# Optimization experiments

Measured on AMD Instinct MI355X. Metric: run time of the kernel, lower is better.

The kernel has to match this reference:

```python
import jax, jax.numpy as jnp
import numpy as np

C_CURV = 0.01
K = 20
BALL_EPS = 4e-3  # hyptorch float32 boundary eps


def _e2p(x, c=C_CURV):
    # ToPoincare: expmap0 then project onto the Poincare ball
    sqrt_c = c ** 0.5
    n = jnp.maximum(jnp.linalg.norm(x, axis=-1, keepdims=True), 1e-15)
    y = jnp.tanh(sqrt_c * n) * x / (sqrt_c * n)
    maxnorm = (1.0 - BALL_EPS) / sqrt_c
    ny = jnp.maximum(jnp.linalg.norm(y, axis=-1, keepdims=True), 1e-15)
    return jnp.where(ny > maxnorm, y * (maxnorm / ny), y)


def _mobius_add(x, y, c=C_CURV):
    x2 = jnp.sum(x * x, axis=-1, keepdims=True)
    y2 = jnp.sum(y * y, axis=-1, keepdims=True)
    xy = jnp.sum(x * y, axis=-1, keepdims=True)
    num = (1.0 + 2.0 * c * xy + c * y2) * x + (1.0 - c * x2) * y
    den = 1.0 + 2.0 * c * xy + c * c * x2 * y2
    return num / jnp.maximum(den, 1e-15)


def _knn(x, k):
    # x: (B, C, N); Euclidean negative squared distance, topk indices
    inner = -2.0 * jnp.einsum('bcn,bcm->bnm', x, x)
    xx = jnp.sum(x * x, axis=1)  # (B, N)
    pd = -xx[:, :, None] - inner - xx[:, None, :]
    return jax.lax.top_k(pd, k)[1]  # (B, N, k)


def _graph_feature(x, k=K):
    # x: (B, C, N) -> (B, 2C, N, k)
    idx = _knn(x, k)
    xp = _e2p(jnp.transpose(x, (0, 2, 1)))  # (B, N, C) on Poincare ball
    feat = jax.vmap(lambda xb, ib: xb[ib])(xp, idx)  # (B, N, k, C) gather
    xc = jnp.broadcast_to(xp[:, :, None, :], feat.shape)
    out = jnp.concatenate([_mobius_add(feat, -xc), xc], axis=-1)
    return jnp.transpose(out, (0, 3, 1, 2))


def _bn(x, g, b, axes, eps=1e-5):
    # BatchNorm (training-mode batch statistics), channel axis = 1
    m = jnp.mean(x, axis=axes, keepdims=True)
    v = jnp.mean((x - m) ** 2, axis=axes, keepdims=True)
    shp = [1] * x.ndim
    shp[1] = -1
    return (x - m) / jnp.sqrt(v + eps) * g.reshape(shp) + b.reshape(shp)


def _ln(x, g, b, eps=1e-5):
    m = jnp.mean(x, axis=-1, keepdims=True)
    v = jnp.mean((x - m) ** 2, axis=-1, keepdims=True)
    return (x - m) / jnp.sqrt(v + eps) * g + b


def setup_inputs() -> dict:
    key = jax.random.key(0)
    ks = jax.random.split(key, 8)
    B, N, OUT = 16, 1024, 40
    s = 0.05
    return {
        'x': jax.random.normal(ks[0], (B, N, 3), jnp.float32),
        'conv1_w': jax.random.normal(ks[1], (64, 6), jnp.float32) * s,
        'bn1_g': jnp.ones((64,), jnp.float32), 'bn1_b': jnp.zeros((64,), jnp.float32),
        'conv2_w': jax.random.normal(ks[2], (192, 128), jnp.float32) * s,
        'bn2_g': jnp.ones((192,), jnp.float32), 'bn2_b': jnp.zeros((192,), jnp.float32),
        'conv3_w': jax.random.normal(ks[3], (1024, 256), jnp.float32) * s,
        'bn3_g': jnp.ones((1024,), jnp.float32), 'bn3_b': jnp.zeros((1024,), jnp.float32),
        'fc1_w': jax.random.normal(ks[4], (512, 1024), jnp.float32) * s,
        'fc1_b': jnp.zeros((512,), jnp.float32),
        'ln1_g': jnp.ones((512,), jnp.float32), 'ln1_b': jnp.zeros((512,), jnp.float32),
        'fc2_w': jax.random.normal(ks[5], (256, 512), jnp.float32) * s,
        'fc2_b': jnp.zeros((256,), jnp.float32),
        'ln2_g': jnp.ones((256,), jnp.float32), 'ln2_b': jnp.zeros((256,), jnp.float32),
        'out_w': jax.random.normal(ks[6], (OUT, 256), jnp.float32) * s,
        'out_b': jnp.zeros((OUT,), jnp.float32),
    }


def reference(x, conv1_w, bn1_g, bn1_b, conv2_w, bn2_g, bn2_b,
              conv3_w, bn3_g, bn3_b, fc1_w, fc1_b, ln1_g, ln1_b,
              fc2_w, fc2_b, ln2_g, ln2_b, out_w, out_b):
    xt = jnp.transpose(x, (0, 2, 1))  # (B, 3, N)
    f = _graph_feature(xt)            # (B, 6, N, k)
    h = jnp.einsum('oc,bcnk->bonk', conv1_w, f)
    h = jax.nn.relu(_bn(h, bn1_g, bn1_b, (0, 2, 3)))
    x1 = jnp.max(h, axis=-1)          # (B, 64, N)
    f = _graph_feature(x1)            # (B, 128, N, k)
    h = jnp.einsum('oc,bcnk->bonk', conv2_w, f)
    h = jax.nn.relu(_bn(h, bn2_g, bn2_b, (0, 2, 3)))
    x2 = jnp.max(h, axis=-1)          # (B, 192, N)
    h = jnp.concatenate([x1, x2], axis=1)  # (B, 256, N)
    h = jnp.einsum('oc,bcn->bon', conv3_w, h)
    h = jax.nn.relu(_bn(h, bn3_g, bn3_b, (0, 2)))
    h = jnp.max(h, axis=-1)           # (B, 1024)
    h = jax.nn.relu(_ln(h @ fc1_w.T + fc1_b, ln1_g, ln1_b))
    h = jax.nn.relu(_ln(h @ fc2_w.T + fc2_b, ln2_g, ln2_b))
    logits = h @ out_w.T + out_b      # (B, outdim)
    return jax.nn.log_softmax(logits, axis=1)
```

## Files before the change

kernel.cpp:

```cpp
#include <hip/hip_runtime.h>
#include <math.h>

#define B_ 16
#define N_ 1024
#define KNN 20
#define NPAIR (B_*N_)

typedef __attribute__((ext_vector_type(8))) short bf16x8;
typedef __attribute__((ext_vector_type(4))) float f32x4;

__device__ __forceinline__ unsigned fkey(float f) {
  unsigned u = __float_as_uint(f);
  return (u & 0x80000000u) ? ~u : (u | 0x80000000u);
}
__device__ __forceinline__ float fkeyinv(unsigned u) {
  unsigned b = (u & 0x80000000u) ? (u ^ 0x80000000u) : ~u;
  return __uint_as_float(b);
}
__device__ __forceinline__ unsigned short f2bf(float x) {
  unsigned u = __float_as_uint(x);
  unsigned r = (u + 0x7FFFu + ((u >> 16) & 1u)) >> 16;
  return (unsigned short)r;
}
__device__ __forceinline__ float bf2f(unsigned short u) {
  return __uint_as_float(((unsigned)u) << 16);
}
__device__ __forceinline__ unsigned knnkey(float d, int idx) {
  return (fkey(d) & 0xFFFFFC00u) | (unsigned)(1023 - idx);
}

__device__ __forceinline__ void topk_insert_u32(unsigned (&kl)[KNN], unsigned nk) {
  kl[KNN-1] = nk;
  #pragma unroll
  for (int i = KNN-1; i > 0; i--) {
    unsigned hi = max(kl[i-1], kl[i]);
    unsigned lo = min(kl[i-1], kl[i]);
    kl[i-1] = hi; kl[i] = lo;
  }
}

__global__ void __launch_bounds__(256) k_prep_knn1(const float* __restrict__ x,
        float* __restrict__ xp1, const float* __restrict__ w2, const float* __restrict__ w3,
        unsigned short* __restrict__ w2h, unsigned short* __restrict__ wt3h,
        unsigned* __restrict__ keypart) {
  __shared__ float P[N_*3];
  __shared__ float XX[N_];
  if (blockIdx.x >= 512) {
    int i = (blockIdx.x - 512) * 256 + threadIdx.x;
    if (i < NPAIR) {
      float a0 = x[i*3+0], a1 = x[i*3+1], a2 = x[i*3+2];
      float n = sqrtf(a0*a0 + a1*a1 + a2*a2);
      n = fmaxf(n, 1e-15f);
      float th = tanhf(0.1f * n);
      float sc = th / (0.1f * n);
      float ny = fmaxf(th * 10.0f, 1e-15f);
      float mxn = (1.0f - 4e-3f) / 0.1f;
      if (ny > mxn) sc *= mxn / ny;
      xp1[i*3+0] = sc*a0; xp1[i*3+1] = sc*a1; xp1[i*3+2] = sc*a2;
    }
    if (i < 192*128) w2h[i] = f2bf(w2[i]);
    wt3h[i] = f2bf(w3[i]);
    return;
  }
  int blk = blockIdx.x;
  int b = blk >> 5, rc = (blk >> 3) & 3, cc = blk & 7;
  const float* xb = x + b*N_*3;
  for (int e = threadIdx.x; e < N_*3; e += 256) P[e] = xb[e];
  __syncthreads();
  for (int j = threadIdx.x; j < N_; j += 256) {
    float q0 = P[j*3], q1 = P[j*3+1], q2 = P[j*3+2];
    XX[j] = q0*q0 + q1*q1 + q2*q2;
  }
  __syncthreads();
  int r = rc*256 + threadIdx.x;
  float q0 = P[r*3], q1 = P[r*3+1], q2 = P[r*3+2];
  float xxq = XX[r];
  unsigned kl[KNN];
  #pragma unroll
  for (int i = 0; i < KNN; i++) kl[i] = 0u;
  int cbase = cc*128;
  for (int jj = 0; jj < 128; jj++) {
    int j = cbase + jj;
    float dot = q0*P[j*3] + q1*P[j*3+1] + q2*P[j*3+2];
    float d = 2.0f*dot - xxq - XX[j];
    unsigned nk = knnkey(d, j);
    if (nk > kl[KNN-1]) topk_insert_u32(kl, nk);
  }
  int p = b*N_ + r;
  unsigned* pe = keypart + (size_t)p*160 + cc*20;
  #pragma unroll
  for (int i = 0; i < KNN; i++) pe[i] = kl[i];
}

__global__ void __launch_bounds__(256) k_conv1(const float* __restrict__ xp1,
                        const unsigned* __restrict__ keypart,
                        const float* __restrict__ w1, float* __restrict__ hmax1,
                        float* __restrict__ hmin1, double* __restrict__ stats1sh) {
  __shared__ float F[4][KNN][6];
  __shared__ float red[4][64][2];
  __shared__ int idxs[16][KNN];
  __shared__ unsigned keybuf[2560];
  int g = threadIdx.x >> 6, lane = threadIdx.x & 63;
  int pbase = blockIdx.x * 16;
  {
    const unsigned* src = keypart + (size_t)pbase*160;
    for (int e = threadIdx.x; e < 2560; e += 256) keybuf[e] = src[e];
  }
  float w[6];
  #pragma unroll
  for (int c = 0; c < 6; c++) w[c] = w1[lane*6 + c];
  __syncthreads();
  if (threadIdx.x < 16) {
    const unsigned* pe = keybuf + threadIdx.x*160;
    int pos[8];
    #pragma unroll
    for (int c = 0; c < 8; c++) pos[c] = 0;
    for (int t = 0; t < KNN; t++) {
      unsigned best = 0u; int bc = 0;
      #pragma unroll
      for (int c = 0; c < 8; c++) {
        if (pos[c] < KNN) {
          unsigned v = pe[c*20 + pos[c]];
          if (v > best) { best = v; bc = c; }
        }
      }
      idxs[threadIdx.x][t] = 1023 - (int)(best & 1023u);
      #pragma unroll
      for (int c = 0; c < 8; c++) if (bc == c) pos[c]++;
    }
  }
  float sum = 0.f, sumsq = 0.f;
  __syncthreads();
  for (int it = 0; it < 4; ++it) {
    int p = pbase + it*4 + g;
    if (lane < KNN) {
      int nb = idxs[it*4 + g][lane];
      int bb = p >> 10;
      const float* xc = xp1 + p*3;
      const float* ft = xp1 + (bb*N_ + nb)*3;
      float x0 = ft[0], x1 = ft[1], x2v = ft[2];
      float c0 = xc[0], c1 = xc[1], c2 = xc[2];
      float X2 = x0*x0 + x1*x1 + x2v*x2v;
      float Y2 = c0*c0 + c1*c1 + c2*c2;
      float XY = -(x0*c0 + x1*c1 + x2v*c2);
      float den = fmaxf(1.0f + 0.02f*XY + 1e-4f*X2*Y2, 1e-15f);
      float s1 = (1.0f + 0.02f*XY + 0.01f*Y2) / den;
      float s2 = (1.0f - 0.01f*X2) / den;
      F[g][lane][0] = s1*x0 - s2*c0;
      F[g][lane][1] = s1*x1 - s2*c1;
      F[g][lane][2] = s1*x2v - s2*c2;
      F[g][lane][3] = c0; F[g][lane][4] = c1; F[g][lane][5] = c2;
    }
    __syncthreads();
    float mx = -__builtin_inff(), mn = __builtin_inff();
    for (int k = 0; k < KNN; k++) {
      float h = 0.f;
      #pragma unroll
      for (int c = 0; c < 6; c++) h = fmaf(w[c], F[g][k][c], h);
      mx = fmaxf(mx, h); mn = fminf(mn, h);
      sum += h; sumsq += h*h;
    }
    hmax1[(pbase + it*4 + g)*64 + lane] = mx;
    hmin1[(pbase + it*4 + g)*64 + lane] = mn;
    __syncthreads();
  }
  red[g][lane][0] = sum; red[g][lane][1] = sumsq;
  __syncthreads();
  if (g == 0) {
    float s  = red[0][lane][0] + red[1][lane][0] + red[2][lane][0] + red[3][lane][0];
    float s2 = red[0][lane][1] + red[1][lane][1] + red[2][lane][1] + red[3][lane][1];
    double* dst = stats1sh + ((size_t)(blockIdx.x & 63)*64 + lane)*2;
    atomicAdd(dst, (double)s);
    atomicAdd(dst + 1, (double)s2);
  }
}

__global__ void __launch_bounds__(64) k_bn_reduce(const double* __restrict__ sh, int nch, double cnt,
                            const float* __restrict__ g, const float* __restrict__ bb,
                            float* __restrict__ scale, float* __restrict__ shift) {
  int o = blockIdx.x, t = threadIdx.x;
  double s  = sh[((size_t)t*nch + o)*2];
  double s2 = sh[((size_t)t*nch + o)*2 + 1];
  #pragma unroll
  for (int off = 32; off > 0; off >>= 1) { s += __shfl_xor(s, off); s2 += __shfl_xor(s2, off); }
  if (t == 0) {
    double m = s / cnt;
    double v = s2 / cnt - m*m;
    float a = g[o] / sqrtf((float)v + 1e-5f);
    scale[o] = a;
    shift[o] = bb[o] - a * (float)m;
  }
}

__global__ void __launch_bounds__(256) k_bn1_apply(const float* __restrict__ hmax1, const float* __restrict__ hmin1,
                            const float* __restrict__ scale1, const float* __restrict__ shift1,
                            float* __restrict__ xp2,
                            unsigned short* __restrict__ x1h, unsigned short* __restrict__ x1l,
                            float* __restrict__ xx1) {
  int b = blockIdx.x >> 4, nc = blockIdx.x & 15;
  int c = threadIdx.x & 63, sub = threadIdx.x >> 6;
  int n0 = nc*64 + sub*16;
  float a = scale1[c], t = shift1[c];
  #pragma unroll
  for (int i = 0; i < 16; i++) {
    int p = b*1024 + n0 + i;
    float h = (a >= 0.f) ? hmax1[(size_t)p*64 + c] : hmin1[(size_t)p*64 + c];
    float x1 = fmaxf(fmaf(a, h, t), 0.f);
    unsigned short hb = f2bf(x1);
    x1h[(size_t)p*64 + c] = hb;
    x1l[(size_t)p*64 + c] = f2bf(x1 - bf2f(hb));
    float n2 = x1*x1;
    #pragma unroll
    for (int off = 32; off > 0; off >>= 1) n2 += __shfl_xor(n2, off);
    if (c == 0) xx1[p] = n2;
    float n1 = fmaxf(sqrtf(n2), 1e-15f);
    float th = tanhf(0.1f * n1);
    float sc = th / (0.1f * n1);
    float ny = fmaxf(th * 10.0f, 1e-15f);
    float mxn = (1.0f - 4e-3f) / 0.1f;
    if (ny > mxn) sc *= mxn / ny;
    xp2[(size_t)p*64 + c] = sc * x1;
  }
}

__global__ void __launch_bounds__(256) k_knn2g(const unsigned short* __restrict__ x1h,
        const unsigned short* __restrict__ x1l,
        const float* __restrict__ xx1, unsigned* __restrict__ keypart2) {
  __shared__ __align__(16) float SM[4096];
  int tid = threadIdx.x;
  int bi = blockIdx.x;
  int blk = ((bi & 7) << 7) + (bi >> 3);
  int b = blk >> 6, qc = (blk >> 2) & 15, cc = blk & 3;
  int qbase = qc*64, ccbase = cc*256;
  int wave = tid >> 6, lane = tid & 63;
  int lm = lane & 15, kq = lane >> 4;
  const size_t base = (size_t)b * 65536;

  bf16x8 Qh[4][2], Ql[4][2];
  #pragma unroll
  for (int qt = 0; qt < 4; qt++) {
    size_t ro = base + (size_t)(qbase + qt*16 + lm)*64 + kq*8;
    #pragma unroll
    for (int ks = 0; ks < 2; ks++) {
      Qh[qt][ks] = *((const bf16x8*)(x1h + ro + ks*32));
      Ql[qt][ks] = *((const bf16x8*)(x1l + ro + ks*32));
    }
  }
  unsigned kl[KNN];
  #pragma unroll
  for (int i = 0; i < KNN; i++) kl[i] = 0u;
  int cq = lane + (lane >> 2);

  for (int st = 0; st < 4; ++st) {
    int cb0 = ccbase + st*64;
    size_t co = base + (size_t)(cb0 + wave*16 + lm)*64 + kq*8;
    bf16x8 Ah[2], Al[2];
    #pragma unroll
    for (int ks = 0; ks < 2; ks++) {
      Ah[ks] = *((const bf16x8*)(x1h + co + ks*32));
      Al[ks] = *((const bf16x8*)(x1l + co + ks*32));
    }
    float4 xxc = *((const float4*)(xx1 + b*1024 + cb0 + wave*16 + kq*4));
    f32x4 acc[4];
    #pragma unroll
    for (int qt = 0; qt < 4; qt++) acc[qt] = (f32x4){0.f, 0.f, 0.f, 0.f};
    #pragma unroll
    for (int ks = 0; ks < 2; ks++) {
      #pragma unroll
      for (int qt = 0; qt < 4; qt++) {
        acc[qt] = __builtin_amdgcn_mfma_f32_16x16x32_bf16(Ah[ks], Qh[qt][ks], acc[qt], 0, 0, 0);
        acc[qt] = __builtin_amdgcn_mfma_f32_16x16x32_bf16(Ah[ks], Ql[qt][ks], acc[qt], 0, 0, 0);
        acc[qt] = __builtin_amdgcn_mfma_f32_16x16x32_bf16(Al[ks], Qh[qt][ks], acc[qt], 0, 0, 0);
        acc[qt] = __builtin_amdgcn_mfma_f32_16x16x32_bf16(Al[ks], Ql[qt][ks], acc[qt], 0, 0, 0);
      }
    }
    __syncthreads();
    float xxcv[4] = {xxc.x, xxc.y, xxc.z, xxc.w};
    #pragma unroll
    for (int qt = 0; qt < 4; qt++) {
      int q = qt*16 + lm;
      #pragma unroll
      for (int r = 0; r < 4; r++) {
        int c = wave*16 + kq*4 + r;
        SM[q*64 + ((c + q + (q>>2)) & 63)] = 2.0f*acc[qt][r] - xxcv[r];
      }
    }
    __syncthreads();
    #pragma unroll
    for (int j = 0; j < 16; j++) {
      int c = wave*16 + j;
      float d = SM[lane*64 + ((c + cq) & 63)];
      unsigned nk = knnkey(d, cb0 + c);
      if (nk > kl[KNN-1]) topk_insert_u32(kl, nk);
    }
  }
  __syncthreads();
  unsigned* U = (unsigned*)SM;
  unsigned* L0 = U;
  unsigned* L1 = U + 1344;
  unsigned* M  = U + 2688;
  if (wave == 0) {
    #pragma unroll
    for (int i = 0; i < KNN; i++) L0[lane*21 + i] = kl[i];
  } else if (wave == 1) {
    #pragma unroll
    for (int i = 0; i < KNN; i++) L1[lane*21 + i] = kl[i];
  }
  __syncthreads();
  if (tid < 64) {
    int ia = 0, ib = 0;
    for (int t = 0; t < KNN; t++) {
      unsigned pa = L0[tid*21 + ia], pb = L1[tid*21 + ib];
      bool ta = pa > pb;
      M[tid*21 + t] = ta ? pa : pb;
      if (ta) ia++; else ib++;
    }
  }
  __syncthreads();
  if (wave == 2) {
    #pragma unroll
    for (int i = 0; i < KNN; i++) L0[lane*21 + i] = kl[i];
  } else if (wave == 3) {
    #pragma unroll
    for (int i = 0; i < KNN; i++) L1[lane*21 + i] = kl[i];
  }
  __syncthreads();
  if (tid < 64) {
    int p = b*N_ + qbase + tid;
    unsigned* pe = keypart2 + (size_t)p*80 + cc*20;
    int ia = 0, ib = 0, im = 0;
    for (int t = 0; t < KNN; t++) {
      unsigned pa = L0[tid*21 + ia], pb = L1[tid*21 + ib], pm = M[tid*21 + im];
      unsigned bp = pm; int sel = 2;
      if (pa > bp) { bp = pa; sel = 0; }
      if (pb > bp) { bp = pb; sel = 1; }
      pe[t] = bp;
      if (sel == 0) ia++; else if (sel == 1) ib++; else im++;
    }
  }
}

__global__ void __launch_bounds__(256) k_conv2m(const float* __restrict__ xp2,
    const unsigned* __restrict__ keypart2, const unsigned short* __restrict__ w2h,
    float* __restrict__ hmax2, float* __restrict__ hmin2, double* __restrict__ stats2sh) {
  __shared__ __align__(16) short Abf[80*136];
  __shared__ int nbr[80];
  __shared__ unsigned keybuf[320];
  int tid = threadIdx.x;
  int bi = blockIdx.x;
  int g512 = ((bi & 7) << 9) + (bi >> 3);
  int p0 = g512 * 4;
  int b = p0 >> 10;
  for (int e = tid; e < 320; e += 256) keybuf[e] = keypart2[(size_t)p0*80 + e];
  __syncthreads();
  if (tid < 4) {
    const unsigned* pe = keybuf + tid*80;
    int pos[4];
    #pragma unroll
    for (int c = 0; c < 4; c++) pos[c] = 0;
    for (int t = 0; t < KNN; t++) {
      unsigned best = 0u; int bc = 0;
      #pragma unroll
      for (int c = 0; c < 4; c++) {
        if (pos[c] < KNN) {
          unsigned v = pe[c*20 + pos[c]];
          if (v > best) { best = v; bc = c; }
        }
      }
      nbr[tid*20 + t] = 1023 - (int)(best & 1023u);
      #pragma unroll
      for (int c = 0; c < 4; c++) if (bc == c) pos[c]++;
    }
  }
  __syncthreads();
  for (int e = tid; e < 80*16; e += 256) {
    int r = e >> 4, qq = e & 15;
    int q = (r >> 2) & 3;
    int L = 20*q + 4*(r >> 4) + (r & 3);
    float4 f = *((const float4*)(xp2 + (size_t)(b*N_ + nbr[L])*64) + qq);
    float4 cv = *((const float4*)(xp2 + (size_t)(p0 + q)*64) + qq);
    float X2 = f.x*f.x + f.y*f.y + f.z*f.z + f.w*f.w;
    float Y2 = cv.x*cv.x + cv.y*cv.y + cv.z*cv.z + cv.w*cv.w;
    float XY = -(f.x*cv.x + f.y*cv.y + f.z*cv.z + f.w*cv.w);
    #pragma unroll
    for (int off = 8; off > 0; off >>= 1) {
      X2 += __shfl_xor(X2, off);
      Y2 += __shfl_xor(Y2, off);
      XY += __shfl_xor(XY, off);
    }
    float den = fmaxf(1.0f + 0.02f*XY + 1e-4f*X2*Y2, 1e-15f);
    float s1 = (1.0f + 0.02f*XY + 0.01f*Y2) / den;
    float s2 = (1.0f - 0.01f*X2) / den;
    ushort4 mo, cb;
    mo.x = f2bf(s1*f.x - s2*cv.x);
    mo.y = f2bf(s1*f.y - s2*cv.y);
    mo.z = f2bf(s1*f.z - s2*cv.z);
    mo.w = f2bf(s1*f.w - s2*cv.w);
    cb.x = f2bf(cv.x); cb.y = f2bf(cv.y); cb.z = f2bf(cv.z); cb.w = f2bf(cv.w);
    *((ushort4*)(Abf + r*136 + qq*4)) = mo;
    *((ushort4*)(Abf + r*136 + 64 + qq*4)) = cb;
  }
  __syncthreads();
  int wave = tid >> 6, lane = tid & 63;
  int quad = lane >> 4, lm = lane & 15;
  int colbase = wave*48;
  f32x4 acc[5][3];
  #pragma unroll
  for (int rt = 0; rt < 5; rt++)
    #pragma unroll
    for (int cj = 0; cj < 3; cj++) acc[rt][cj] = (f32x4){0.f, 0.f, 0.f, 0.f};
  #pragma unroll
  for (int kt = 0; kt < 4; kt++) {
    int k0 = kt*32 + quad*8;
    bf16x8 bf[3];
    #pragma unroll
    for (int cj = 0; cj < 3; cj++)
      bf[cj] = *((const bf16x8*)(w2h + (size_t)(colbase + cj*16 + lm)*128 + k0));
    bf16x8 af[5];
    #pragma unroll
    for (int rt = 0; rt < 5; rt++)
      af[rt] = *((const bf16x8*)(Abf + (rt*16 + lm)*136 + k0));
    #pragma unroll
    for (int rt = 0; rt < 5; rt++)
      #pragma unroll
      for (int cj = 0; cj < 3; cj++)
        acc[rt][cj] = __builtin_amdgcn_mfma_f32_16x16x32_bf16(af[rt], bf[cj], acc[rt][cj], 0, 0, 0);
  }
  #pragma unroll
  for (int cj = 0; cj < 3; cj++) {
    int o = colbase + cj*16 + lm;
    float s = 0.f, s2 = 0.f, mx = -__builtin_inff(), mn = __builtin_inff();
    #pragma unroll
    for (int rt = 0; rt < 5; rt++) {
      #pragma unroll
      for (int reg = 0; reg < 4; reg++) {
        float h = acc[rt][cj][reg];
        s += h; s2 += h*h;
        mx = fmaxf(mx, h); mn = fminf(mn, h);
      }
    }
    hmax2[(size_t)(p0 + quad)*192 + o] = mx;
    hmin2[(size_t)(p0 + quad)*192 + o] = mn;
    s  += __shfl_xor(s, 16);  s  += __shfl_xor(s, 32);
    s2 += __shfl_xor(s2, 16); s2 += __shfl_xor(s2, 32);
    if (lane < 16) {
      double* dst = stats2sh + ((size_t)(bi & 63)*192 + o)*2;
      atomicAdd(dst, (double)s); atomicAdd(dst + 1, (double)s2);
    }
  }
}

__global__ void __launch_bounds__(256) k_conv3m(
   const float* __restrict__ hmax1, const float* __restrict__ hmin1,
   const float* __restrict__ scale1, const float* __restrict__ shift1,
   const float* __restrict__ hmax2, const float* __restrict__ hmin2,
   const float* __restrict__ scale2, const float* __restrict__ shift2,
   const unsigned short* __restrict__ wt3h, double* __restrict__ stats3sh,
   unsigned* __restrict__ hmax3u, unsigned* __restrict__ hmin3u) {
  __shared__ short As[64*264];
  int tid = threadIdx.x;
  int mt = blockIdx.x >> 2, cb = blockIdx.x & 3;
  int rowbase = mt*64;
  int b = rowbase >> 10;
  int c4 = tid & 63;
  float4 sc, sh;
  if (c4 < 16) {
    sc = *((const float4*)(scale1 + c4*4));
    sh = *((const float4*)(shift1 + c4*4));
  } else {
    sc = *((const float4*)(scale2 + (c4*4 - 64)));
    sh = *((const float4*)(shift2 + (c4*4 - 64)));
  }
  #pragma unroll 4
  for (int i = 0; i < 16; i++) {
    int r = (tid >> 6) + i*4;
    int p = rowbase + r;
    float4 hx, hn;
    if (c4 < 16) {
      hx = *((const float4*)(hmax1 + (size_t)p*64 + c4*4));
      hn = *((const float4*)(hmin1 + (size_t)p*64 + c4*4));
    } else {
      hx = *((const float4*)(hmax2 + (size_t)p*192 + (c4*4 - 64)));
      hn = *((const float4*)(hmin2 + (size_t)p*192 + (c4*4 - 64)));
    }
    ushort4 o4;
    o4.x = f2bf(fmaxf(fmaf(sc.x, (sc.x >= 0.f ? hx.x : hn.x), sh.x), 0.f));
    o4.y = f2bf(fmaxf(fmaf(sc.y, (sc.y >= 0.f ? hx.y : hn.y), sh.y), 0.f));
    o4.z = f2bf(fmaxf(fmaf(sc.z, (sc.z >= 0.f ? hx.z : hn.z), sh.z), 0.f));
    o4.w = f2bf(fmaxf(fmaf(sc.w, (sc.w >= 0.f ? hx.w : hn.w), sh.w), 0.f));
    *((ushort4*)(As + r*264 + c4*4)) = o4;
  }
  __syncthreads();
  int wave = tid >> 6, lane = tid & 63;
  int quad = lane >> 4, lm = lane & 15;
  int colbase = cb*256 + wave*64;
  f32x4 acc[4][4];
  #pragma unroll
  for (int ri = 0; ri < 4; ri++)
    #pragma unroll
    for (int cj = 0; cj < 4; cj++) acc[ri][cj] = (f32x4){0.f, 0.f, 0.f, 0.f};
  for (int kt = 0; kt < 8; kt++) {
    int k0 = kt*32 + quad*8;
    bf16x8 bf[4];
    #pragma unroll
    for (int cj = 0; cj < 4; cj++)
      bf[cj] = *((const bf16x8*)(wt3h + (size_t)(colbase + cj*16 + lm)*256 + k0));
    bf16x8 af[4];
    #pragma unroll
    for (int ri = 0; ri < 4; ri++)
      af[ri] = *((const bf16x8*)(As + (ri*16 + lm)*264 + k0));
    #pragma unroll
    for (int ri = 0; ri < 4; ri++)
      #pragma unroll
      for (int cj = 0; cj < 4; cj++)
        acc[ri][cj] = __builtin_amdgcn_mfma_f32_16x16x32_bf16(af[ri], bf[cj], acc[ri][cj], 0, 0, 0);
  }
  #pragma unroll
  for (int cj = 0; cj < 4; cj++) {
    float s = 0.f, s2 = 0.f, mx = -__builtin_inff(), mn = __builtin_inff();
    #pragma unroll
    for (int ri = 0; ri < 4; ri++) {
      #pragma unroll
      for (int reg = 0; reg < 4; reg++) {
        float h = acc[ri][cj][reg];
        s += h; s2 += h*h; mx = fmaxf(mx, h); mn = fminf(mn, h);
      }
    }
    s  += __shfl_xor(s, 16);  s  += __shfl_xor(s, 32);
    s2 += __shfl_xor(s2, 16); s2 += __shfl_xor(s2, 32);
    mx = fmaxf(mx, __shfl_xor(mx, 16)); mx = fmaxf(mx, __shfl_xor(mx, 32));
    mn = fminf(mn, __shfl_xor(mn, 16)); mn = fminf(mn, __shfl_xor(mn, 32));
    if (lane < 16) {
      int col = colbase + cj*16 + lane;
      double* dst = stats3sh + ((size_t)(blockIdx.x & 63)*1024 + col)*2;
      atomicAdd(dst, (double)s);
      atomicAdd(dst + 1, (double)s2);
      atomicMax(hmax3u + b*1024 + col, fkey(mx));
      atomicMin(hmin3u + b*1024 + col, fkey(mn));
    }
  }
}

__device__ float blk_reduce(float v, float* red, int tid) {
  red[tid] = v; __syncthreads();
  for (int st = 128; st > 0; st >>= 1) {
    if (tid < st) red[tid] += red[tid + st];
    __syncthreads();
  }
  float r = red[0]; __syncthreads();
  return r;
}

__global__ void __launch_bounds__(256) k_head1(const unsigned* __restrict__ hmax3u,
    const unsigned* __restrict__ hmin3u,
    const float* __restrict__ scale3, const float* __restrict__ shift3,
    const float* __restrict__ fc1w, const float* __restrict__ fc1b,
    float* __restrict__ h1buf) {
  __shared__ __align__(16) float V[1024];
  int b = blockIdx.x >> 5, oc = blockIdx.x & 31;
  int tid = threadIdx.x;
  for (int o = tid; o < 1024; o += 256) {
    float a = scale3[o];
    unsigned u = (a >= 0.f) ? hmax3u[b*1024 + o] : hmin3u[b*1024 + o];
    V[o] = fmaxf(fmaf(a, fkeyinv(u), shift3[o]), 0.f);
  }
  __syncthreads();
  int ty = tid >> 4, tx = tid & 15;
  int o = oc*16 + ty;
  const float4* wr = (const float4*)(fc1w + (size_t)o*1024) + tx*16;
  const float4* vv = (const float4*)V + tx*16;
  float s = 0.f;
  #pragma unroll
  for (int i = 0; i < 16; i++) {
    float4 w = wr[i]; float4 v = vv[i];
    s = fmaf(w.x, v.x, s); s = fmaf(w.y, v.y, s);
    s = fmaf(w.z, v.z, s); s = fmaf(w.w, v.w, s);
  }
  s += __shfl_xor(s, 1); s += __shfl_xor(s, 2);
  s += __shfl_xor(s, 4); s += __shfl_xor(s, 8);
  if (tx == 0) h1buf[b*512 + o] = s + fc1b[o];
}

__global__ void __launch_bounds__(256) k_head2(const float* __restrict__ h1buf,
    const float* __restrict__ ln1g, const float* __restrict__ ln1b,
    const float* __restrict__ fc2w, const float* __restrict__ fc2b,
    float* __restrict__ h2buf) {
  __shared__ __align__(16) float H1[512];
  __shared__ float red[256];
  int b = blockIdx.x >> 3, oc = blockIdx.x & 7;
  int tid = threadIdx.x;
  float v0 = h1buf[b*512 + tid], v1 = h1buf[b*512 + 256 + tid];
  float s = blk_reduce(v0 + v1, red, tid);
  float s2 = blk_reduce(v0*v0 + v1*v1, red, tid);
  float m = s / 512.f;
  float var = s2 / 512.f - m*m;
  float inv = 1.0f / sqrtf(var + 1e-5f);
  H1[tid] = fmaxf((v0 - m)*inv*ln1g[tid] + ln1b[tid], 0.f);
  H1[256 + tid] = fmaxf((v1 - m)*inv*ln1g[256 + tid] + ln1b[256 + tid], 0.f);
  __syncthreads();
  int ty = tid >> 3, tx = tid & 7;
  int o = oc*32 + ty;
  const float4* wr = (const float4*)(fc2w + (size_t)o*512) + tx*16;
  const float4* vv = (const float4*)H1 + tx*16;
  float t = 0.f;
  #pragma unroll
  for (int i = 0; i < 16; i++) {
    float4 w = wr[i]; float4 v = vv[i];
    t = fmaf(w.x, v.x, t); t = fmaf(w.y, v.y, t);
    t = fmaf(w.z, v.z, t); t = fmaf(w.w, v.w, t);
  }
  t += __shfl_xor(t, 1); t += __shfl_xor(t, 2); t += __shfl_xor(t, 4);
  if (tx == 0) h2buf[b*256 + o] = t + fc2b[o];
}

__global__ void __launch_bounds__(256) k_head3(const float* __restrict__ h2buf,
    const float* __restrict__ ln2g, const float* __restrict__ ln2b,
    const float* __restrict__ outw, const float* __restrict__ outb,
    float* __restrict__ out) {
  __shared__ __align__(16) float H2[256];
  __shared__ float red[256];
  int b = blockIdx.x, tid = threadIdx.x;
  float h2v = h2buf[b*256 + tid];
  float ss = blk_reduce(h2v, red, tid);
  float ss2 = blk_reduce(h2v*h2v, red, tid);
  float m2 = ss / 256.f;
  float var2 = ss2 / 256.f - m2*m2;
  float inv2 = 1.0f / sqrtf(var2 + 1e-5f);
  H2[tid] = fmaxf((h2v - m2)*inv2*ln2g[tid] + ln2b[tid], 0.f);
  __syncthreads();
  if (tid < 40) {
    const float4* wr = (const float4*)(outw + (size_t)tid*256);
    float t = 0.f;
    for (int c4 = 0; c4 < 64; c4++) {
      float4 w = wr[c4]; float4 vv = ((const float4*)H2)[c4];
      t = fmaf(w.x, vv.x, t); t = fmaf(w.y, vv.y, t);
      t = fmaf(w.z, vv.z, t); t = fmaf(w.w, vv.w, t);
    }
    red[tid] = t + outb[tid];
  }
  __syncthreads();
  if (tid == 0) {
    float mx = -__builtin_inff();
    for (int i2 = 0; i2 < 40; i2++) mx = fmaxf(mx, red[i2]);
    float se = 0.f;
    for (int i2 = 0; i2 < 40; i2++) se += expf(red[i2] - mx);
    float lse = mx + logf(se);
    for (int i2 = 0; i2 < 40; i2++) out[b*40 + i2] = red[i2] - lse;
  }
}

extern "C" void kernel_launch(void* const* d_in, const int* in_sizes, int n_in,
                              void* d_out, int out_size, void* d_ws, size_t ws_size,
                              hipStream_t stream) {
  (void)in_sizes; (void)n_in; (void)out_size; (void)ws_size;
  const float* x    = (const float*)d_in[0];
  const float* w1   = (const float*)d_in[1];
  const float* bn1g = (const float*)d_in[2];
  const float* bn1b = (const float*)d_in[3];
  const float* w2   = (const float*)d_in[4];
  const float* bn2g = (const float*)d_in[5];
  const float* bn2b = (const float*)d_in[6];
  const float* w3   = (const float*)d_in[7];
  const float* bn3g = (const float*)d_in[8];
  const float* bn3b = (const float*)d_in[9];
  const float* fc1w = (const float*)d_in[10];
  const float* fc1b = (const float*)d_in[11];
  const float* ln1g = (const float*)d_in[12];
  const float* ln1b = (const float*)d_in[13];
  const float* fc2w = (const float*)d_in[14];
  const float* fc2b = (const float*)d_in[15];
  const float* ln2g = (const float*)d_in[16];
  const float* ln2b = (const float*)d_in[17];
  const float* outw = (const float*)d_in[18];
  const float* outb = (const float*)d_in[19];
  float* out = (float*)d_out;

  float* ws = (float*)d_ws;
  size_t off = 0;
  float* xp1   = ws + off; off += 49152;
  float* hmax1 = ws + off; off += 1048576;
  float* hmin1 = ws + off; off += 1048576;
  float* xp2   = ws + off; off += 1048576;
  float* hmax2 = ws + off; off += 3145728;
  float* hmin2 = ws + off; off += 3145728;
  unsigned* keypart2 = (unsigned*)(ws + off); off += 1310720;
  unsigned short* w2h = (unsigned short*)(ws + off); off += 24576;
  unsigned short* wt3h = (unsigned short*)(ws + off); off += 131072;
  float* x1bf  = ws + off; off += 1048576;
  float* xx1   = ws + off; off += 16384;
  float* h1buf = ws + off; off += 8192;
  float* h2buf = ws + off; off += 4096;
  float* scale1 = ws + off; off += 64;
  float* shift1 = ws + off; off += 64;
  float* scale2 = ws + off; off += 192;
  float* shift2 = ws + off; off += 192;
  float* scale3 = ws + off; off += 1024;
  float* shift3 = ws + off; off += 1024;
  double* stats1sh = (double*)(ws + off);
  double* stats2sh = stats1sh + 64*64*2;
  double* stats3sh = stats2sh + 64*192*2;
  unsigned* hmax3u = (unsigned*)(stats3sh + (size_t)64*1024*2);
  unsigned* hmin3u = hmax3u + 16384;
  unsigned* keypartA = (unsigned*)hmax2;
  unsigned short* x1h = (unsigned short*)x1bf;
  unsigned short* x1l = x1h + 1048576;

  size_t zero_bytes = ((size_t)64*64*2 + (size_t)64*192*2 + (size_t)64*1024*2)*8 + (size_t)16384*4;
  hipMemsetAsync(stats1sh, 0, zero_bytes, stream);
  hipMemsetAsync(hmin3u, 0xFF, (size_t)16384*4, stream);

  k_prep_knn1<<<1536, 256, 0, stream>>>(x, xp1, w2, w3, w2h, wt3h, keypartA);
  k_conv1<<<1024, 256, 0, stream>>>(xp1, keypartA, w1, hmax1, hmin1, stats1sh);
  k_bn_reduce<<<64, 64, 0, stream>>>(stats1sh, 64, 327680.0, bn1g, bn1b, scale1, shift1);
  k_bn1_apply<<<256, 256, 0, stream>>>(hmax1, hmin1, scale1, shift1, xp2, x1h, x1l, xx1);
  k_knn2g<<<1024, 256, 0, stream>>>(x1h, x1l, xx1, keypart2);
  k_conv2m<<<4096, 256, 0, stream>>>(xp2, keypart2, w2h, hmax2, hmin2, stats2sh);
  k_bn_reduce<<<192, 64, 0, stream>>>(stats2sh, 192, 327680.0, bn2g, bn2b, scale2, shift2);
  k_conv3m<<<1024, 256, 0, stream>>>(hmax1, hmin1, scale1, shift1, hmax2, hmin2, scale2, shift2,
                                     wt3h, stats3sh, hmax3u, hmin3u);
  k_bn_reduce<<<1024, 64, 0, stream>>>(stats3sh, 1024, 16384.0, bn3g, bn3b, scale3, shift3);
  k_head1<<<512, 256, 0, stream>>>(hmax3u, hmin3u, scale3, shift3, fc1w, fc1b, h1buf);
  k_head2<<<128, 256, 0, stream>>>(h1buf, ln1g, ln1b, fc2w, fc2b, h2buf);
  k_head3<<<16, 256, 0, stream>>>(h2buf, ln2g, ln2b, outw, outb, out);
}
```

Before: 371.2 us.

## Parallelize neighbor merge by rank counting and spread conv2 stats atomics

Replaces the serial 4-thread merge of per-chunk top-k lists in k_conv2m with a parallel rank computation, where each candidate binary-searches the other sorted chunks and writes itself directly to its merged slot. The center-point bf16 copy and its squared norm are computed once per point and reused from shared memory instead of being recomputed for every neighbor row. The division becomes a refined reciprocal. BN2 statistics atomics are spread over 256 slots instead of 64 to reduce contention, and k_bn_reduce now loops over a configurable slot count. The center vector used in the Mobius add is now bf16-rounded, which slightly changes numerics.

After: 365.2 us. No clear change (-1.6%).

```diff
diff --git a/kernel.cpp b/kernel.cpp
--- a/kernel.cpp
+++ b/kernel.cpp
@@ -175,12 +175,16 @@
   }
 }
 
-__global__ void __launch_bounds__(64) k_bn_reduce(const double* __restrict__ sh, int nch, double cnt,
+__global__ void __launch_bounds__(64) k_bn_reduce(const double* __restrict__ sh, int nch, int nslots,
+                            double cnt,
                             const float* __restrict__ g, const float* __restrict__ bb,
                             float* __restrict__ scale, float* __restrict__ shift) {
   int o = blockIdx.x, t = threadIdx.x;
-  double s  = sh[((size_t)t*nch + o)*2];
-  double s2 = sh[((size_t)t*nch + o)*2 + 1];
+  double s = 0.0, s2 = 0.0;
+  for (int sl = t; sl < nslots; sl += 64) {
+    s  += sh[((size_t)sl*nch + o)*2];
+    s2 += sh[((size_t)sl*nch + o)*2 + 1];
+  }
   #pragma unroll
   for (int off = 32; off > 0; off >>= 1) { s += __shfl_xor(s, off); s2 += __shfl_xor(s2, off); }
   if (t == 0) {
@@ -344,6 +348,7 @@
     const unsigned* __restrict__ keypart2, const unsigned short* __restrict__ w2h,
     float* __restrict__ hmax2, float* __restrict__ hmin2, double* __restrict__ stats2sh) {
   __shared__ __align__(16) short Abf[80*136];
+  __shared__ float Yc[4];
   __shared__ int nbr[80];
   __shared__ unsigned keybuf[320];
   int tid = threadIdx.x;
@@ -352,25 +357,43 @@
   int p0 = g512 * 4;
   int b = p0 >> 10;
   for (int e = tid; e < 320; e += 256) keybuf[e] = keypart2[(size_t)p0*80 + e];
-  __syncthreads();
-  if (tid < 4) {
-    const unsigned* pe = keybuf + tid*80;
-    int pos[4];
-    #pragma unroll
-    for (int c = 0; c < 4; c++) pos[c] = 0;
-    for (int t = 0; t < KNN; t++) {
-      unsigned best = 0u; int bc = 0;
-      #pragma unroll
-      for (int c = 0; c < 4; c++) {
-        if (pos[c] < KNN) {
-          unsigned v = pe[c*20 + pos[c]];
-          if (v > best) { best = v; bc = c; }
-        }
+  if (tid < 64) {
+    int pt = tid >> 4, qq = tid & 15;
+    float4 cv = *((const float4*)(xp2 + (size_t)(p0 + pt)*64) + qq);
+    float y2 = cv.x*cv.x + cv.y*cv.y + cv.z*cv.z + cv.w*cv.w;
+    #pragma unroll
+    for (int off = 8; off > 0; off >>= 1) y2 += __shfl_xor(y2, off);
+    if (qq == 0) Yc[pt] = y2;
+    ushort4 cb;
+    cb.x = f2bf(cv.x); cb.y = f2bf(cv.y); cb.z = f2bf(cv.z); cb.w = f2bf(cv.w);
+    #pragma unroll
+    for (int a = 0; a < 5; a++)
+      #pragma unroll
+      for (int j2 = 0; j2 < 4; j2++)
+        *((ushort4*)(Abf + (a*16 + pt*4 + j2)*136 + 64 + qq*4)) = cb;
+  }
+  __syncthreads();
+  for (int e = tid; e < 320; e += 256) {
+    int pt = e / 80;
+    int rem = e - pt*80;
+    int c = rem / 20;
+    int i = rem - c*20;
+    const unsigned* LB = keybuf + pt*80;
+    unsigned v = LB[c*20 + i];
+    int rank = i;
+    #pragma unroll
+    for (int c2 = 0; c2 < 4; c2++) {
+      if (c2 == c) continue;
+      const unsigned* Lp = LB + c2*20;
+      int j = 0;
+      #pragma unroll
+      for (int s = 16; s; s >>= 1) {
+        int nj = j + s;
+        if (nj <= KNN && Lp[nj-1] > v) j = nj;
       }
-      nbr[tid*20 + t] = 1023 - (int)(best & 1023u);
-      #pragma unroll
-      for (int c = 0; c < 4; c++) if (bc == c) pos[c]++;
-    }
+      rank += j;
+    }
+    if (rank < KNN) nbr[pt*20 + rank] = 1023 - (int)(v & 1023u);
   }
   __syncthreads();
   for (int e = tid; e < 80*16; e += 256) {
@@ -378,27 +401,27 @@
     int q = (r >> 2) & 3;
     int L = 20*q + 4*(r >> 4) + (r & 3);
     float4 f = *((const float4*)(xp2 + (size_t)(b*N_ + nbr[L])*64) + qq);
-    float4 cv = *((const float4*)(xp2 + (size_t)(p0 + q)*64) + qq);
+    ushort4 cb4 = *((const ushort4*)(Abf + r*136 + 64 + qq*4));
+    float c0 = bf2f(cb4.x), c1 = bf2f(cb4.y), c2v = bf2f(cb4.z), c3 = bf2f(cb4.w);
     float X2 = f.x*f.x + f.y*f.y + f.z*f.z + f.w*f.w;
-    float Y2 = cv.x*cv.x + cv.y*cv.y + cv.z*cv.z + cv.w*cv.w;
-    float XY = -(f.x*cv.x + f.y*cv.y + f.z*cv.z + f.w*cv.w);
+    float XY = -(f.x*c0 + f.y*c1 + f.z*c2v + f.w*c3);
     #pragma unroll
     for (int off = 8; off > 0; off >>= 1) {
       X2 += __shfl_xor(X2, off);
-      Y2 += __shfl_xor(Y2, off);
       XY += __shfl_xor(XY, off);
     }
+    float Y2 = Yc[q];
     float den = fmaxf(1.0f + 0.02f*XY + 1e-4f*X2*Y2, 1e-15f);
-    float s1 = (1.0f + 0.02f*XY + 0.01f*Y2) / den;
-    float s2 = (1.0f - 0.01f*X2) / den;
-    ushort4 mo, cb;
-    mo.x = f2bf(s1*f.x - s2*cv.x);
-    mo.y = f2bf(s1*f.y - s2*cv.y);
-    mo.z = f2bf(s1*f.z - s2*cv.z);
-    mo.w = f2bf(s1*f.w - s2*cv.w);
-    cb.x = f2bf(cv.x); cb.y = f2bf(cv.y); cb.z = f2bf(cv.z); cb.w = f2bf(cv.w);
+    float rc = __builtin_amdgcn_rcpf(den);
+    rc = rc * (2.0f - den*rc);
+    float s1 = (1.0f + 0.02f*XY + 0.01f*Y2) * rc;
+    float s2 = (1.0f - 0.01f*X2) * rc;
+    ushort4 mo;
+    mo.x = f2bf(s1*f.x - s2*c0);
+    mo.y = f2bf(s1*f.y - s2*c1);
+    mo.z = f2bf(s1*f.z - s2*c2v);
+    mo.w = f2bf(s1*f.w - s2*c3);
     *((ushort4*)(Abf + r*136 + qq*4)) = mo;
-    *((ushort4*)(Abf + r*136 + 64 + qq*4)) = cb;
   }
   __syncthreads();
   int wave = tid >> 6, lane = tid & 63;
@@ -444,7 +467,7 @@
     s  += __shfl_xor(s, 16);  s  += __shfl_xor(s, 32);
     s2 += __shfl_xor(s2, 16); s2 += __shfl_xor(s2, 32);
     if (lane < 16) {
-      double* dst = stats2sh + ((size_t)(bi & 63)*192 + o)*2;
+      double* dst = stats2sh + ((size_t)(bi & 255)*192 + o)*2;
       atomicAdd(dst, (double)s); atomicAdd(dst + 1, (double)s2);
     }
   }
@@ -698,27 +721,27 @@
   float* shift3 = ws + off; off += 1024;
   double* stats1sh = (double*)(ws + off);
   double* stats2sh = stats1sh + 64*64*2;
-  double* stats3sh = stats2sh + 64*192*2;
+  double* stats3sh = stats2sh + (size_t)256*192*2;
   unsigned* hmax3u = (unsigned*)(stats3sh + (size_t)64*1024*2);
   unsigned* hmin3u = hmax3u + 16384;
   unsigned* keypartA = (unsigned*)hmax2;
   unsigned short* x1h = (unsigned short*)x1bf;
   unsigned short* x1l = x1h + 1048576;
 
-  size_t zero_bytes = ((size_t)64*64*2 + (size_t)64*192*2 + (size_t)64*1024*2)*8 + (size_t)16384*4;
+  size_t zero_bytes = ((size_t)64*64*2 + (size_t)256*192*2 + (size_t)64*1024*2)*8 + (size_t)16384*4;
   hipMemsetAsync(stats1sh, 0, zero_bytes, stream);
   hipMemsetAsync(hmin3u, 0xFF, (size_t)16384*4, stream);
 
   k_prep_knn1<<<1536, 256, 0, stream>>>(x, xp1, w2, w3, w2h, wt3h, keypartA);
   k_conv1<<<1024, 256, 0, stream>>>(xp1, keypartA, w1, hmax1, hmin1, stats1sh);
-  k_bn_reduce<<<64, 64, 0, stream>>>(stats1sh, 64, 327680.0, bn1g, bn1b, scale1, shift1);
+  k_bn_reduce<<<64, 64, 0, stream>>>(stats1sh, 64, 64, 327680.0, bn1g, bn1b, scale1, shift1);
   k_bn1_apply<<<256, 256, 0, stream>>>(hmax1, hmin1, scale1, shift1, xp2, x1h, x1l, xx1);
   k_knn2g<<<1024, 256, 0, stream>>>(x1h, x1l, xx1, keypart2);
   k_conv2m<<<4096, 256, 0, stream>>>(xp2, keypart2, w2h, hmax2, hmin2, stats2sh);
-  k_bn_reduce<<<192, 64, 0, stream>>>(stats2sh, 192, 327680.0, bn2g, bn2b, scale2, shift2);
+  k_bn_reduce<<<192, 64, 0, stream>>>(stats2sh, 192, 256, 327680.0, bn2g, bn2b, scale2, shift2);
   k_conv3m<<<1024, 256, 0, stream>>>(hmax1, hmin1, scale1, shift1, hmax2, hmin2, scale2, shift2,
                                      wt3h, stats3sh, hmax3u, hmin3u);
-  k_bn_reduce<<<1024, 64, 0, stream>>>(stats3sh, 1024, 16384.0, bn3g, bn3b, scale3, shift3);
+  k_bn_reduce<<<1024, 64, 0, stream>>>(stats3sh, 1024, 64, 16384.0, bn3g, bn3b, scale3, shift3);
   k_head1<<<512, 256, 0, stream>>>(hmax3u, hmin3u, scale3, shift3, fc1w, fc1b, h1buf);
   k_head2<<<128, 256, 0, stream>>>(h1buf, ln1g, ln1b, fc2w, fc2b, h2buf);
   k_head3<<<16, 256, 0, stream>>>(h2buf, ln2g, ln2b, outw, outb, out);
```
